# Kernel optimization log

Hardware: AMD Instinct MI355X
Metric: run time of the kernel (lower is better)

The kernel has to match this reference:

```python
import jax, jax.numpy as jnp
import numpy as np

B, T0, T1, WIDTH, N, K, H = 1, 512, 1536, 2048, 16, 4, 128
T = T0 + T1
THETA = 1000000.0
ROT = H // 2          # partial_rotary_factor = 0.5 -> rotary dim 64
EPS = 1e-6
NEG = -2.3819763e38


def _rmsnorm(x, scale):
    var = jnp.mean(jnp.square(x.astype(jnp.float32)), axis=-1, keepdims=True)
    normed = x * jnp.reciprocal(jnp.sqrt(var + EPS))
    return (normed * (1.0 + scale)).astype(x.dtype)


def _rope(x, cos, sin):
    # x: [B,T,n,H]; rotate first ROT dims (rotate-half convention), pass-through rest
    xr, xp = x[..., :ROT], x[..., ROT:]
    x1, x2 = jnp.split(xr, 2, axis=-1)
    rot = jnp.concatenate([x1 * cos - x2 * sin, x2 * cos + x1 * sin], axis=-1)
    return jnp.concatenate([rot, xp], axis=-1)


def _stream(x, tm, qg_w, k_w, v_w, qn, kn):
    x = x * tm[..., None].astype(x.dtype)
    qg = jnp.einsum('btd,ndh->btnh', x, qg_w)     # [B,t,N,2H]
    q, gate = jnp.split(qg, 2, axis=-1)
    q = _rmsnorm(q, qn)
    k = _rmsnorm(jnp.einsum('btd,kdh->btkh', x, k_w), kn)
    v = jnp.einsum('btd,kdh->btkh', x, v_w)
    return q, k, v, gate


def setup_inputs():
    key = jax.random.key(0)
    ks = jax.random.split(key, 10)
    f = jnp.float32
    sd = WIDTH ** -0.5
    so = (N * H) ** -0.5
    inp = {}
    inp['x0'] = jax.random.normal(ks[0], (B, T0, WIDTH), f)
    inp['x1'] = jax.random.normal(ks[1], (B, T1, WIDTH), f)
    inp['positions'] = jnp.broadcast_to(jnp.arange(T, dtype=jnp.int32), (B, T))
    inp['attn_mask'] = jnp.broadcast_to(jnp.tril(jnp.ones((T, T), bool)), (B, T, T))
    inp['qg_w0'] = jax.random.normal(ks[2], (N, WIDTH, 2 * H), f) * sd
    inp['k_w0'] = jax.random.normal(ks[3], (K, WIDTH, H), f) * sd
    inp['v_w0'] = jax.random.normal(ks[4], (K, WIDTH, H), f) * sd
    inp['qn0'] = jnp.zeros((H,), f)
    inp['kn0'] = jnp.zeros((H,), f)
    inp['o_w0'] = jax.random.normal(ks[5], (N, H, WIDTH), f) * so
    inp['qg_w1'] = jax.random.normal(ks[6], (N, WIDTH, 2 * H), f) * sd
    inp['k_w1'] = jax.random.normal(ks[7], (K, WIDTH, H), f) * sd
    inp['v_w1'] = jax.random.normal(ks[8], (K, WIDTH, H), f) * sd
    inp['qn1'] = jnp.zeros((H,), f)
    inp['kn1'] = jnp.zeros((H,), f)
    inp['o_w1'] = jax.random.normal(ks[9], (N, H, WIDTH), f) * so
    return inp


def reference(x0, x1, positions, attn_mask,
              qg_w0, k_w0, v_w0, qn0, kn0, o_w0,
              qg_w1, k_w1, v_w1, qn1, kn1, o_w1):
    token_mask = jnp.any(attn_mask, axis=-1)  # [B,T]
    q0, k0, v0, g0 = _stream(x0, token_mask[:, :T0], qg_w0, k_w0, v_w0, qn0, kn0)
    q1, k1, v1, g1 = _stream(x1, token_mask[:, T0:], qg_w1, k_w1, v_w1, qn1, kn1)
    q = jnp.concatenate([q0, q1], axis=1)      # [B,T,N,H]
    k = jnp.concatenate([k0, k1], axis=1)      # [B,T,K,H]
    v = jnp.concatenate([v0, v1], axis=1)
    gate = jnp.concatenate([g0, g1], axis=1)

    half = ROT // 2
    inv_freq = THETA ** (-jnp.arange(half, dtype=jnp.float32) / half)
    ang = positions.astype(jnp.float32)[:, :, None] * inv_freq   # [B,T,half]
    cos = jnp.cos(ang)[:, :, None, :]
    sin = jnp.sin(ang)[:, :, None, :]
    q = _rope(q, cos, sin)
    k = _rope(k, cos, sin)
    q = q * (H ** -0.5)

    cached_k, cached_v = k, v                  # kv_cache is None (prefill)
    rep = N // K
    k = jnp.repeat(k, rep, axis=2)             # [B,T,N,H]
    v = jnp.repeat(v, rep, axis=2)

    mask = attn_mask[:, None, :, :]            # [B,1,T,S]
    logits = jnp.einsum('btnh,bsnh->bnts', q, k, preferred_element_type=jnp.float32)
    masked = jnp.where(mask, logits, NEG)
    probs = jax.nn.softmax(masked, axis=-1).astype(q.dtype)
    probs = probs * jnp.any(mask, axis=-1, keepdims=True).astype(q.dtype)
    enc = jnp.einsum('bnts,bsnh->btnh', probs, v)
    enc = enc * jax.nn.sigmoid(gate).astype(enc.dtype)
    out0 = jnp.einsum('btnh,nhd->btd', enc[:, :T0], o_w0)
    out1 = jnp.einsum('btnh,nhd->btd', enc[:, T0:], o_w1)
    return (out0, out1, cached_k, cached_v)
```

## Files before the change

kernel.cpp:

```cpp
#include <hip/hip_runtime.h>
#include <hip/hip_bf16.h>
#include <cstdint>
#include <cstddef>

#define T0_ 512
#define TT_ 2048
#define WD_ 2048
#define NH_ 16
#define KH_ 4

typedef __attribute__((ext_vector_type(8))) short short8;
typedef __attribute__((ext_vector_type(4))) short short4v;
typedef __attribute__((ext_vector_type(4))) float f32x4;

#define AS1 __attribute__((address_space(1)))
#define AS3 __attribute__((address_space(3)))

__device__ __forceinline__ ushort f2bf(float x) {
  __hip_bfloat16 h = __float2bfloat16(x);
  ushort u; __builtin_memcpy(&u, &h, 2); return u;
}
__device__ __forceinline__ float bf2f(ushort u) {
  __hip_bfloat16 h; __builtin_memcpy(&h, &u, 2);
  return __bfloat162float(h);
}
__device__ __forceinline__ void g2l16(const ushort* g, AS3 ushort* s) {
  __builtin_amdgcn_global_load_lds((const AS1 uint32_t*)g, (AS3 uint32_t*)s, 16, 0, 0);
}

__global__ __launch_bounds__(256) void convert_x(
    const float* __restrict__ x0, const float* __restrict__ x1, ushort* __restrict__ xb)
{
  const int i = blockIdx.x * 256 + threadIdx.x;
  const int e = i * 4;
  const int row = e >> 11, col = e & 2047;
  const float* src = (row < T0_) ? (x0 + (size_t)row * WD_ + col)
                                 : (x1 + (size_t)(row - T0_) * WD_ + col);
  const float4 v = *(const float4*)src;
  ushort4 o; o.x = f2bf(v.x); o.y = f2bf(v.y); o.z = f2bf(v.z); o.w = f2bf(v.w);
  *(ushort4*)(xb + e) = o;
}

__global__ __launch_bounds__(256) void convtrans64(
    const float* __restrict__ s0, const float* __restrict__ s1,
    ushort* __restrict__ d0, ushort* __restrict__ d1, int R, int C, int half)
{
  __shared__ float tile[64][67];
  int z = blockIdx.z;
  const float* in; ushort* out;
  if (z < half) { in = s0 + (size_t)z * R * C; out = d0 + (size_t)z * R * C; }
  else { z -= half; in = s1 + (size_t)z * R * C; out = d1 + (size_t)z * R * C; }
  const int r0 = blockIdx.x * 64, c0 = blockIdx.y * 64;
  const int cx = threadIdx.x & 15, ry = threadIdx.x >> 4;
#pragma unroll
  for (int i = 0; i < 4; ++i) {
    const int r = ry + i * 16;
    const float4 v = *(const float4*)&in[(size_t)(r0 + r) * C + c0 + cx * 4];
    tile[cx * 4 + 0][r] = v.x;
    tile[cx * 4 + 1][r] = v.y;
    tile[cx * 4 + 2][r] = v.z;
    tile[cx * 4 + 3][r] = v.w;
  }
  __syncthreads();
  const int rq = threadIdx.x & 15, cy = threadIdx.x >> 4;
#pragma unroll
  for (int i = 0; i < 4; ++i) {
    const int c = cy + i * 16;
    ushort4 o;
    o.x = f2bf(tile[c][rq * 4 + 0]);
    o.y = f2bf(tile[c][rq * 4 + 1]);
    o.z = f2bf(tile[c][rq * 4 + 2]);
    o.w = f2bf(tile[c][rq * 4 + 3]);
    *(ushort4*)&out[(size_t)(c0 + c) * R + r0 + rq * 4] = o;
  }
}

__device__ __forceinline__ void gemm_core(
    const ushort* __restrict__ A, const ushort* __restrict__ Bt,
    int row0, int col0, ushort* As, ushort* Bs, f32x4 (&acc)[4][4])
{
  const int tid = threadIdx.x;
  const int w = tid >> 6, l = tid & 63, lq = l >> 4, lm = l & 15;
  const int wr = (w >> 1) * 64, wc = (w & 1) * 64;
  const int sx = lm & 7;
  const int gsw = (tid & 7) ^ ((tid >> 3) & 7);
  const ushort* Ag = A + (size_t)(row0 + (tid >> 3)) * WD_ + gsw * 8;
  const ushort* Bg = Bt + (size_t)(col0 + (tid >> 3)) * WD_ + gsw * 8;
  AS3 ushort* AsW = (AS3 ushort*)As + w * 512;
  AS3 ushort* BsW = (AS3 ushort*)Bs + w * 512;

  auto stage = [&](int buf, int k0) {
#pragma unroll
    for (int c = 0; c < 4; ++c) {
      g2l16(Ag + (size_t)(c * 32) * WD_ + k0, AsW + buf * 8192 + c * 2048);
      g2l16(Bg + (size_t)(c * 32) * WD_ + k0, BsW + buf * 8192 + c * 2048);
    }
  };

  stage(0, 0);
  __syncthreads();
  int buf = 0;
  for (int k0 = 0; k0 < WD_; k0 += 64) {
    if (k0 + 64 < WD_) stage(buf ^ 1, k0 + 64);
    const ushort* Ab = As + buf * 8192;
    const ushort* Bb = Bs + buf * 8192;
#pragma unroll
    for (int kk = 0; kk < 2; ++kk) {
      short8 af[4], bfr[4];
#pragma unroll
      for (int mi = 0; mi < 4; ++mi)
        af[mi] = *(const short8*)&Ab[(wr + mi * 16 + lm) * 64 + (((kk * 4 + lq) ^ sx) << 3)];
#pragma unroll
      for (int ni = 0; ni < 4; ++ni)
        bfr[ni] = *(const short8*)&Bb[(wc + ni * 16 + lm) * 64 + (((kk * 4 + lq) ^ sx) << 3)];
#pragma unroll
      for (int mi = 0; mi < 4; ++mi)
#pragma unroll
        for (int ni = 0; ni < 4; ++ni)
          acc[mi][ni] = __builtin_amdgcn_mfma_f32_16x16x32_bf16(af[mi], bfr[ni], acc[mi][ni], 0, 0, 0);
    }
    __syncthreads();
    buf ^= 1;
  }
}

__global__ __launch_bounds__(256) void gemm_proj(
    const ushort* __restrict__ A,
    const ushort* __restrict__ qg0t, const ushort* __restrict__ qg1t,
    const ushort* __restrict__ k0t,  const ushort* __restrict__ k1t,
    const ushort* __restrict__ v0t,  const ushort* __restrict__ v1t,
    ushort* __restrict__ Cqg, float* __restrict__ kc, float* __restrict__ vc)
{
  __shared__ ushort As[16384], Bs[16384];
  const int bx = blockIdx.x;
  const int row0 = blockIdx.y * 128;
  const bool s1 = (row0 >= T0_);
  const ushort* Bt; int col0;
  float* Cf = nullptr; ushort* Cb = nullptr; int ldc;
  if (bx < 32) {
    Bt = s1 ? qg1t : qg0t; col0 = bx * 128; Cb = Cqg; ldc = 4096;
  } else if (bx < 36) {
    Bt = s1 ? k1t : k0t; col0 = (bx - 32) * 128; Cf = kc; ldc = 512;
  } else {
    Bt = s1 ? v1t : v0t; col0 = (bx - 36) * 128; Cf = vc; ldc = 512;
  }
  f32x4 acc[4][4];
#pragma unroll
  for (int mi = 0; mi < 4; ++mi)
#pragma unroll
    for (int ni = 0; ni < 4; ++ni) acc[mi][ni] = (f32x4){0.f, 0.f, 0.f, 0.f};
  gemm_core(A, Bt, row0, col0, As, Bs, acc);
  const int w = threadIdx.x >> 6, l = threadIdx.x & 63, lq = l >> 4, lm = l & 15;
  const int wr = (w >> 1) * 64, wc = (w & 1) * 64;
#pragma unroll
  for (int mi = 0; mi < 4; ++mi)
#pragma unroll
    for (int ni = 0; ni < 4; ++ni)
#pragma unroll
      for (int r = 0; r < 4; ++r) {
        const size_t rr = (size_t)row0 + wr + mi * 16 + lq * 4 + r;
        const size_t cc = (size_t)col0 + wc + ni * 16 + lm;
        if (Cb) Cb[rr * ldc + cc] = f2bf(acc[mi][ni][r]);
        else    Cf[rr * ldc + cc] = acc[mi][ni][r];
      }
}

__global__ __launch_bounds__(256) void gemm_out(
    const ushort* __restrict__ A, const ushort* __restrict__ W0t,
    const ushort* __restrict__ W1t, float* __restrict__ C)
{
  __shared__ ushort As[16384], Bs[16384];
  const int row0 = blockIdx.y * 128, col0 = blockIdx.x * 128;
  const ushort* Bt = (row0 < T0_) ? W0t : W1t;
  f32x4 acc[4][4];
#pragma unroll
  for (int mi = 0; mi < 4; ++mi)
#pragma unroll
    for (int ni = 0; ni < 4; ++ni) acc[mi][ni] = (f32x4){0.f, 0.f, 0.f, 0.f};
  gemm_core(A, Bt, row0, col0, As, Bs, acc);
  const int w = threadIdx.x >> 6, l = threadIdx.x & 63, lq = l >> 4, lm = l & 15;
  const int wr = (w >> 1) * 64, wc = (w & 1) * 64;
#pragma unroll
  for (int mi = 0; mi < 4; ++mi)
#pragma unroll
    for (int ni = 0; ni < 4; ++ni)
#pragma unroll
      for (int r = 0; r < 4; ++r) {
        const size_t rr = (size_t)row0 + wr + mi * 16 + lq * 4 + r;
        const size_t cc = (size_t)col0 + wc + ni * 16 + lm;
        C[rr * 2048 + cc] = acc[mi][ni][r];
      }
}

__global__ __launch_bounds__(256) void postproc_vt(
    ushort* __restrict__ qgb, float* __restrict__ kc, ushort* __restrict__ Kb,
    const int* __restrict__ positions,
    const float* __restrict__ qn0, const float* __restrict__ kn0,
    const float* __restrict__ qn1, const float* __restrict__ kn1,
    const float* __restrict__ vcache, ushort* __restrict__ Vtb)
{
  __shared__ float tile[64][67];
  if (blockIdx.x >= 2048) {
    const int idx = blockIdx.x - 2048;
    const int r0 = (idx & 31) * 64, c0 = (idx >> 5) * 64;
    const int cx = threadIdx.x & 15, ry = threadIdx.x >> 4;
#pragma unroll
    for (int i = 0; i < 4; ++i) {
      const int r = ry + i * 16;
      const float4 v = *(const float4*)&vcache[(size_t)(r0 + r) * 512 + c0 + cx * 4];
      tile[cx * 4 + 0][r] = v.x;
      tile[cx * 4 + 1][r] = v.y;
      tile[cx * 4 + 2][r] = v.z;
      tile[cx * 4 + 3][r] = v.w;
    }
    __syncthreads();
    const int rq = threadIdx.x & 15, cy = threadIdx.x >> 4;
#pragma unroll
    for (int i = 0; i < 4; ++i) {
      const int c = cy + i * 16;
      ushort4 o;
      o.x = f2bf(tile[c][rq * 4 + 0]);
      o.y = f2bf(tile[c][rq * 4 + 1]);
      o.z = f2bf(tile[c][rq * 4 + 2]);
      o.w = f2bf(tile[c][rq * 4 + 3]);
      *(ushort4*)&Vtb[(size_t)(c0 + c) * 2048 + r0 + rq * 4] = o;
    }
    return;
  }
  const int t = blockIdx.x;
  const int w = threadIdx.x >> 6, l = threadIdx.x & 63;
  const float pos = (float)positions[t];
  const bool str1 = (t >= T0_);
  const float* qn = str1 ? qn1 : qn0;
  const float* kn = str1 ? kn1 : kn0;
  const float kfreq = 13.815510557964274f / 32.0f;
  const int h0 = 2 * l, h1 = 2 * l + 1;

  for (int r = w; r < NH_ + KH_; r += 4) {
    const bool isq = (r < NH_);
    float v0, v1; size_t bi; const float* sc;
    if (isq) {
      bi = ((size_t)t * NH_ + r) * 256;
      v0 = bf2f(qgb[bi + h0]); v1 = bf2f(qgb[bi + h1]); sc = qn;
    } else {
      bi = ((size_t)t * KH_ + (r - NH_)) * 128;
      v0 = kc[bi + h0]; v1 = kc[bi + h1]; sc = kn;
    }
    float ss = v0 * v0 + v1 * v1;
#pragma unroll
    for (int off = 32; off > 0; off >>= 1) ss += __shfl_xor(ss, off);
    const float rstd = rsqrtf(ss * (1.0f / 128.0f) + 1e-6f);
    v0 = v0 * rstd * (1.0f + sc[h0]);
    v1 = v1 * rstd * (1.0f + sc[h1]);
    const float p0 = __shfl_xor(v0, 16);
    const float p1 = __shfl_xor(v1, 16);
    if (l < 32) {
      const int i0 = (l < 16) ? h0 : (h0 - 32);
      const float a0 = pos * __expf(-(float)i0 * kfreq);
      const float a1 = pos * __expf(-(float)(i0 + 1) * kfreq);
      const float c0 = cosf(a0), s0 = sinf(a0);
      const float c1 = cosf(a1), s1v = sinf(a1);
      if (l < 16) { v0 = v0 * c0 - p0 * s0; v1 = v1 * c1 - p1 * s1v; }
      else        { v0 = v0 * c0 + p0 * s0; v1 = v1 * c1 + p1 * s1v; }
    }
    if (isq) {
      v0 *= 0.08838834764831843f; v1 *= 0.08838834764831843f;
      qgb[bi + h0] = f2bf(v0); qgb[bi + h1] = f2bf(v1);
    } else {
      kc[bi + h0] = v0; kc[bi + h1] = v1;
      Kb[bi + h0] = f2bf(v0); Kb[bi + h1] = f2bf(v1);
    }
  }
}

__global__ __launch_bounds__(256) void attn(
    const ushort* __restrict__ qgb, const ushort* __restrict__ Kb,
    const ushort* __restrict__ Vt, ushort* __restrict__ encb)
{
  __shared__ ushort Ks[2 * 8192];
  __shared__ ushort Vs[2 * 8192];
  __shared__ ushort Ps[4 * 1024];
  const int tid = threadIdx.x;
  const int w = tid >> 6, l = tid & 63, lq = l >> 4, lm = l & 15;
  const int n = blockIdx.y, kh = n >> 2;
  const int qt = (n < 8) ? (int)blockIdx.x : (31 - (int)blockIdx.x);
  const int qtb = qt * 64;
  const int nst = qt + 1;

  auto stage = [&](int buf, int s0) {
#pragma unroll
    for (int c = 0; c < 4; ++c) {
      {
        const int base = c * 16 + w * 4;
        const int row = base + (l >> 4);
        const int j = l & 15;
        g2l16(Kb + (size_t)(s0 + row) * 512 + kh * 128 + (j ^ (row & 15)) * 8,
              (AS3 ushort*)Ks + buf * 8192 + base * 128);
      }
      {
        const int base = c * 32 + w * 8;
        const int row = base + (l >> 3);
        const int j = l & 7;
        g2l16(Vt + (size_t)(kh * 128 + row) * 2048 + s0 + (j ^ (row & 7)) * 8,
              (AS3 ushort*)Vs + buf * 8192 + base * 64);
      }
    }
  };

  short8 aq[4];
  {
    const ushort* qb = qgb + ((size_t)(qtb + w * 16 + lm) * NH_ + n) * 256 + lq * 8;
#pragma unroll
    for (int kk = 0; kk < 4; ++kk) aq[kk] = *(const short8*)(qb + kk * 32);
  }
  f32x4 acc[8];
#pragma unroll
  for (int i = 0; i < 8; ++i) acc[i] = (f32x4){0.f, 0.f, 0.f, 0.f};
  float mq = -3.0e38f, lsum = 0.0f;

  stage(0, 0);

  for (int st = 0; st < nst; ++st) {
    const int buf = st & 1;
    const int s0 = st * 64;
    __syncthreads();
    if (st + 1 < nst) stage(buf ^ 1, s0 + 64);
    const ushort* Kt = Ks + buf * 8192;
    const ushort* Vb = Vs + buf * 8192;

    f32x4 sa[4];
#pragma unroll
    for (int mi = 0; mi < 4; ++mi) sa[mi] = (f32x4){0.f, 0.f, 0.f, 0.f};
#pragma unroll
    for (int kk = 0; kk < 4; ++kk)
#pragma unroll
      for (int mi = 0; mi < 4; ++mi) {
        const short8 ak = *(const short8*)&Kt[(mi * 16 + lm) * 128 + ((kk * 4 + lq) ^ lm) * 8];
        sa[mi] = __builtin_amdgcn_mfma_f32_16x16x32_bf16(ak, aq[kk], sa[mi], 0, 0, 0);
      }
    if (s0 + 63 > qtb) {
      const int qg_ = qtb + w * 16 + lm;
#pragma unroll
      for (int mi = 0; mi < 4; ++mi)
#pragma unroll
        for (int r = 0; r < 4; ++r)
          if (s0 + mi * 16 + lq * 4 + r > qg_) sa[mi][r] = -3.0e38f;
    }
    float mx = sa[0][0];
#pragma unroll
    for (int mi = 0; mi < 4; ++mi)
#pragma unroll
      for (int r = 0; r < 4; ++r) mx = fmaxf(mx, sa[mi][r]);
    mx = fmaxf(mx, __shfl_xor(mx, 16));
    mx = fmaxf(mx, __shfl_xor(mx, 32));
    const float mn = fmaxf(mq, mx);
    const float alpha = __expf(mq - mn);
    mq = mn;
    float sl = 0.0f;
#pragma unroll
    for (int mi = 0; mi < 4; ++mi)
#pragma unroll
      for (int r = 0; r < 4; ++r) {
        const float p = __expf(sa[mi][r] - mn);
        sa[mi][r] = p; sl += p;
      }
    sl += __shfl_xor(sl, 16);
    sl += __shfl_xor(sl, 32);
    lsum = lsum * alpha + sl;

#pragma unroll
    for (int mi = 0; mi < 4; ++mi) {
      short4v pw;
#pragma unroll
      for (int r = 0; r < 4; ++r) pw[r] = (short)f2bf(sa[mi][r]);
      *(short4v*)&Ps[w * 1024 + lm * 64 + ((mi * 4 + lq) ^ lm) * 4] = pw;
    }
    float aP[4];
#pragma unroll
    for (int r = 0; r < 4; ++r) aP[r] = __shfl(alpha, lq * 4 + r);
#pragma unroll
    for (int hi = 0; hi < 8; ++hi) {
      f32x4 a = acc[hi];
#pragma unroll
      for (int r = 0; r < 4; ++r) a[r] *= aP[r];
      acc[hi] = a;
    }
#pragma unroll
    for (int mi2 = 0; mi2 < 2; ++mi2) {
      const short4v pa = *(const short4v*)&Ps[w * 1024 + lm * 64 + ((mi2 * 8 + lq * 2 + 0) ^ lm) * 4];
      const short4v pb = *(const short4v*)&Ps[w * 1024 + lm * 64 + ((mi2 * 8 + lq * 2 + 1) ^ lm) * 4];
      const short8 ap = __builtin_shufflevector(pa, pb, 0, 1, 2, 3, 4, 5, 6, 7);
#pragma unroll
      for (int hi = 0; hi < 8; ++hi) {
        const short8 bv = *(const short8*)&Vb[(hi * 16 + lm) * 64 + (((mi2 * 4 + lq) ^ (lm & 7)) << 3)];
        acc[hi] = __builtin_amdgcn_mfma_f32_16x16x32_bf16(ap, bv, acc[hi], 0, 0, 0);
      }
    }
  }
  const float linv = 1.0f / lsum;
  float lP[4];
#pragma unroll
  for (int r = 0; r < 4; ++r) lP[r] = __shfl(linv, lq * 4 + r);
#pragma unroll
  for (int hi = 0; hi < 8; ++hi)
#pragma unroll
    for (int r = 0; r < 4; ++r) {
      const int t = qtb + w * 16 + lq * 4 + r;
      const int h = hi * 16 + lm;
      const float g = bf2f(qgb[((size_t)t * NH_ + n) * 256 + 128 + h]);
      const float o = acc[hi][r] * lP[r] * (1.0f / (1.0f + __expf(-g)));
      encb[((size_t)t * NH_ + n) * 128 + h] = f2bf(o);
    }
}

extern "C" void kernel_launch(void* const* d_in, const int* in_sizes, int n_in,
                              void* d_out, int out_size, void* d_ws, size_t ws_size,
                              hipStream_t stream)
{
  (void)in_sizes; (void)n_in; (void)out_size; (void)ws_size;
  const float* x0    = (const float*)d_in[0];
  const float* x1    = (const float*)d_in[1];
  const int*   pos   = (const int*)d_in[2];
  const float* qg_w0 = (const float*)d_in[4];
  const float* k_w0  = (const float*)d_in[5];
  const float* v_w0  = (const float*)d_in[6];
  const float* qn0   = (const float*)d_in[7];
  const float* kn0   = (const float*)d_in[8];
  const float* o_w0  = (const float*)d_in[9];
  const float* qg_w1 = (const float*)d_in[10];
  const float* k_w1  = (const float*)d_in[11];
  const float* v_w1  = (const float*)d_in[12];
  const float* qn1   = (const float*)d_in[13];
  const float* kn1   = (const float*)d_in[14];
  const float* o_w1  = (const float*)d_in[15];

  float* out    = (float*)d_out;
  float* kcache = out + (size_t)TT_ * WD_;
  float* vcache = kcache + (size_t)TT_ * KH_ * 128;
  ushort* qsc = (ushort*)d_out;

  ushort* wbuf = (ushort*)d_ws;
  ushort* xb   = wbuf + 8388608;
  ushort* qgb  = xb + 4194304;
  ushort* encb = qgb + 8388608;
  ushort* Kbuf = xb;
  ushort* Vtb  = xb + 1048576;
  ushort* k0t = encb, *k1t = encb + 1048576, *v0t = encb + 2097152, *v1t = encb + 3145728;

  convert_x<<<4096, 256, 0, stream>>>(x0, x1, xb);

  convtrans64<<<dim3(32, 4, 32), 256, 0, stream>>>(qg_w0, qg_w1, qsc, wbuf, WD_, 256, 16);
  convtrans64<<<dim3(32, 2, 8), 256, 0, stream>>>(k_w0, k_w1, k0t, k1t, WD_, 128, 4);
  convtrans64<<<dim3(32, 2, 8), 256, 0, stream>>>(v_w0, v_w1, v0t, v1t, WD_, 128, 4);

  gemm_proj<<<dim3(40, 16), 256, 0, stream>>>(xb, qsc, wbuf, k0t, k1t, v0t, v1t,
                                              qgb, kcache, vcache);

  postproc_vt<<<2304, 256, 0, stream>>>(qgb, kcache, Kbuf, pos, qn0, kn0, qn1, kn1,
                                        vcache, Vtb);

  attn<<<dim3(32, 16), 256, 0, stream>>>(qgb, Kbuf, Vtb, encb);

  convtrans64<<<dim3(32, 32, 2), 256, 0, stream>>>(o_w0, o_w1, wbuf, wbuf + 4194304, WD_, WD_, 1);
  gemm_out<<<dim3(16, 16), 256, 0, stream>>>(encb, wbuf, wbuf + 4194304, out);
}
```

Baseline: 373.8 us.

## Fuse input conversion and weight transposes into one prep kernel; retile output GEMM

```diff
diff --git a/kernel.cpp b/kernel.cpp
--- a/kernel.cpp
+++ b/kernel.cpp
@@ -28,17 +28,68 @@
   __builtin_amdgcn_global_load_lds((const AS1 uint32_t*)g, (AS3 uint32_t*)s, 16, 0, 0);
 }
 
-__global__ __launch_bounds__(256) void convert_x(
-    const float* __restrict__ x0, const float* __restrict__ x1, ushort* __restrict__ xb)
-{
-  const int i = blockIdx.x * 256 + threadIdx.x;
-  const int e = i * 4;
-  const int row = e >> 11, col = e & 2047;
-  const float* src = (row < T0_) ? (x0 + (size_t)row * WD_ + col)
-                                 : (x1 + (size_t)(row - T0_) * WD_ + col);
-  const float4 v = *(const float4*)src;
-  ushort4 o; o.x = f2bf(v.x); o.y = f2bf(v.y); o.z = f2bf(v.z); o.w = f2bf(v.w);
-  *(ushort4*)(xb + e) = o;
+__global__ __launch_bounds__(256) void prep(
+    const float* __restrict__ x0, const float* __restrict__ x1, ushort* __restrict__ xb,
+    const float* __restrict__ qg_w0, const float* __restrict__ qg_w1,
+    ushort* __restrict__ qg0t, ushort* __restrict__ qg1t,
+    const float* __restrict__ k_w0, const float* __restrict__ k_w1,
+    ushort* __restrict__ k0t, ushort* __restrict__ k1t,
+    const float* __restrict__ v_w0, const float* __restrict__ v_w1,
+    ushort* __restrict__ v0t, ushort* __restrict__ v1t)
+{
+  __shared__ float tile[64][67];
+  int b = blockIdx.x;
+  if (b < 4096) {
+    const int i = b * 256 + threadIdx.x;
+    const int e = i * 4;
+    const int row = e >> 11, col = e & 2047;
+    const float* src = (row < T0_) ? (x0 + (size_t)row * WD_ + col)
+                                   : (x1 + (size_t)(row - T0_) * WD_ + col);
+    const float4 v = *(const float4*)src;
+    ushort4 o; o.x = f2bf(v.x); o.y = f2bf(v.y); o.z = f2bf(v.z); o.w = f2bf(v.w);
+    *(ushort4*)(xb + e) = o;
+    return;
+  }
+  b -= 4096;
+  const float* in; ushort* out; int C, rt, ct;
+  if (b < 4096) {
+    const int z = b >> 7, rem = b & 127; rt = rem & 31; ct = rem >> 5; C = 256;
+    if (z < 16) { in = qg_w0 + (size_t)z * WD_ * 256; out = qg0t + (size_t)z * WD_ * 256; }
+    else { in = qg_w1 + (size_t)(z - 16) * WD_ * 256; out = qg1t + (size_t)(z - 16) * WD_ * 256; }
+  } else if (b < 4608) {
+    b -= 4096;
+    const int z = b >> 6, rem = b & 63; rt = rem & 31; ct = rem >> 5; C = 128;
+    if (z < 4) { in = k_w0 + (size_t)z * WD_ * 128; out = k0t + (size_t)z * WD_ * 128; }
+    else { in = k_w1 + (size_t)(z - 4) * WD_ * 128; out = k1t + (size_t)(z - 4) * WD_ * 128; }
+  } else {
+    b -= 4608;
+    const int z = b >> 6, rem = b & 63; rt = rem & 31; ct = rem >> 5; C = 128;
+    if (z < 4) { in = v_w0 + (size_t)z * WD_ * 128; out = v0t + (size_t)z * WD_ * 128; }
+    else { in = v_w1 + (size_t)(z - 4) * WD_ * 128; out = v1t + (size_t)(z - 4) * WD_ * 128; }
+  }
+  const int r0 = rt * 64, c0 = ct * 64;
+  const int cx = threadIdx.x & 15, ry = threadIdx.x >> 4;
+#pragma unroll
+  for (int i = 0; i < 4; ++i) {
+    const int r = ry + i * 16;
+    const float4 v = *(const float4*)&in[(size_t)(r0 + r) * C + c0 + cx * 4];
+    tile[cx * 4 + 0][r] = v.x;
+    tile[cx * 4 + 1][r] = v.y;
+    tile[cx * 4 + 2][r] = v.z;
+    tile[cx * 4 + 3][r] = v.w;
+  }
+  __syncthreads();
+  const int rq = threadIdx.x & 15, cy = threadIdx.x >> 4;
+#pragma unroll
+  for (int i = 0; i < 4; ++i) {
+    const int c = cy + i * 16;
+    ushort4 o;
+    o.x = f2bf(tile[c][rq * 4 + 0]);
+    o.y = f2bf(tile[c][rq * 4 + 1]);
+    o.z = f2bf(tile[c][rq * 4 + 2]);
+    o.w = f2bf(tile[c][rq * 4 + 3]);
+    *(ushort4*)&out[(size_t)(c0 + c) * WD_ + r0 + rq * 4] = o;
+  }
 }
 
 __global__ __launch_bounds__(256) void convtrans64(
@@ -169,21 +220,63 @@
     const ushort* __restrict__ A, const ushort* __restrict__ W0t,
     const ushort* __restrict__ W1t, float* __restrict__ C)
 {
-  __shared__ ushort As[16384], Bs[16384];
-  const int row0 = blockIdx.y * 128, col0 = blockIdx.x * 128;
+  __shared__ ushort As[2 * 8192], Bs[2 * 4096];
+  const int row0 = blockIdx.y * 128, col0 = blockIdx.x * 64;
   const ushort* Bt = (row0 < T0_) ? W0t : W1t;
-  f32x4 acc[4][4];
+  const int tid = threadIdx.x;
+  const int w = tid >> 6, l = tid & 63, lq = l >> 4, lm = l & 15;
+  const int wr = (w >> 1) * 64, wc = (w & 1) * 32;
+  const int sx = lm & 7;
+  const int gsw = (tid & 7) ^ ((tid >> 3) & 7);
+  const ushort* Ag = A + (size_t)(row0 + (tid >> 3)) * WD_ + gsw * 8;
+  const ushort* Bg = Bt + (size_t)(col0 + (tid >> 3)) * WD_ + gsw * 8;
+  AS3 ushort* AsW = (AS3 ushort*)As + w * 512;
+  AS3 ushort* BsW = (AS3 ushort*)Bs + w * 512;
+
+  f32x4 acc[4][2];
 #pragma unroll
   for (int mi = 0; mi < 4; ++mi)
 #pragma unroll
-    for (int ni = 0; ni < 4; ++ni) acc[mi][ni] = (f32x4){0.f, 0.f, 0.f, 0.f};
-  gemm_core(A, Bt, row0, col0, As, Bs, acc);
-  const int w = threadIdx.x >> 6, l = threadIdx.x & 63, lq = l >> 4, lm = l & 15;
-  const int wr = (w >> 1) * 64, wc = (w & 1) * 64;
+    for (int ni = 0; ni < 2; ++ni) acc[mi][ni] = (f32x4){0.f, 0.f, 0.f, 0.f};
+
+  auto stage = [&](int buf, int k0) {
+#pragma unroll
+    for (int c = 0; c < 4; ++c)
+      g2l16(Ag + (size_t)(c * 32) * WD_ + k0, AsW + buf * 8192 + c * 2048);
+#pragma unroll
+    for (int c = 0; c < 2; ++c)
+      g2l16(Bg + (size_t)(c * 32) * WD_ + k0, BsW + buf * 4096 + c * 2048);
+  };
+
+  stage(0, 0);
+  __syncthreads();
+  int buf = 0;
+  for (int k0 = 0; k0 < WD_; k0 += 64) {
+    if (k0 + 64 < WD_) stage(buf ^ 1, k0 + 64);
+    const ushort* Ab = As + buf * 8192;
+    const ushort* Bb = Bs + buf * 4096;
+#pragma unroll
+    for (int kk = 0; kk < 2; ++kk) {
+      short8 af[4], bfr[2];
+#pragma unroll
+      for (int mi = 0; mi < 4; ++mi)
+        af[mi] = *(const short8*)&Ab[(wr + mi * 16 + lm) * 64 + (((kk * 4 + lq) ^ sx) << 3)];
+#pragma unroll
+      for (int ni = 0; ni < 2; ++ni)
+        bfr[ni] = *(const short8*)&Bb[(wc + ni * 16 + lm) * 64 + (((kk * 4 + lq) ^ sx) << 3)];
+#pragma unroll
+      for (int mi = 0; mi < 4; ++mi)
+#pragma unroll
+        for (int ni = 0; ni < 2; ++ni)
+          acc[mi][ni] = __builtin_amdgcn_mfma_f32_16x16x32_bf16(af[mi], bfr[ni], acc[mi][ni], 0, 0, 0);
+    }
+    __syncthreads();
+    buf ^= 1;
+  }
 #pragma unroll
   for (int mi = 0; mi < 4; ++mi)
 #pragma unroll
-    for (int ni = 0; ni < 4; ++ni)
+    for (int ni = 0; ni < 2; ++ni)
 #pragma unroll
       for (int r = 0; r < 4; ++r) {
         const size_t rr = (size_t)row0 + wr + mi * 16 + lq * 4 + r;
@@ -447,11 +540,10 @@
   ushort* Vtb  = xb + 1048576;
   ushort* k0t = encb, *k1t = encb + 1048576, *v0t = encb + 2097152, *v1t = encb + 3145728;
 
-  convert_x<<<4096, 256, 0, stream>>>(x0, x1, xb);
-
-  convtrans64<<<dim3(32, 4, 32), 256, 0, stream>>>(qg_w0, qg_w1, qsc, wbuf, WD_, 256, 16);
-  convtrans64<<<dim3(32, 2, 8), 256, 0, stream>>>(k_w0, k_w1, k0t, k1t, WD_, 128, 4);
-  convtrans64<<<dim3(32, 2, 8), 256, 0, stream>>>(v_w0, v_w1, v0t, v1t, WD_, 128, 4);
+  prep<<<9216, 256, 0, stream>>>(x0, x1, xb,
+                                 qg_w0, qg_w1, qsc, wbuf,
+                                 k_w0, k_w1, k0t, k1t,
+                                 v_w0, v_w1, v0t, v1t);
 
   gemm_proj<<<dim3(40, 16), 256, 0, stream>>>(xb, qsc, wbuf, k0t, k1t, v0t, v1t,
                                               qgb, kcache, vcache);
@@ -462,5 +554,5 @@
   attn<<<dim3(32, 16), 256, 0, stream>>>(qgb, Kbuf, Vtb, encb);
 
   convtrans64<<<dim3(32, 32, 2), 256, 0, stream>>>(o_w0, o_w1, wbuf, wbuf + 4194304, WD_, WD_, 1);
-  gemm_out<<<dim3(16, 16), 256, 0, stream>>>(encb, wbuf, wbuf + 4194304, out);
-}
+  gemm_out<<<dim3(32, 16), 256, 0, stream>>>(encb, wbuf, wbuf + 4194304, out);
+}
```

New measurement: 363.7 us. -2.7%, faster.
